# Optimization experiments

Hardware: AMD Instinct MI355X
Metric: run time of the kernel (lower is better)

The kernel has to match this reference:

```python
import jax, jax.numpy as jnp
import numpy as np

D_MODEL = 1024
H = 16
D_K = D_MODEL // H
NEG = -1.0e9


def setup_inputs() -> dict:
    key = jax.random.key(0)
    ks = jax.random.split(key, 12)
    B, S = 2, 2048
    s = 1.0 / np.sqrt(D_MODEL)
    inp = {
        "q": jax.random.normal(ks[0], (B, S, D_MODEL), jnp.float32),
        "k": jax.random.normal(ks[1], (B, S, D_MODEL), jnp.float32),
        "v": jax.random.normal(ks[2], (B, S, D_MODEL), jnp.float32),
        "mask": jnp.tril(jnp.ones((S, S), jnp.int32))[None, None, :, :],
        "wq": jax.random.normal(ks[3], (D_MODEL, D_MODEL), jnp.float32) * s,
        "bq": jax.random.normal(ks[4], (D_MODEL,), jnp.float32) * s,
        "wk": jax.random.normal(ks[5], (D_MODEL, D_MODEL), jnp.float32) * s,
        "bk": jax.random.normal(ks[6], (D_MODEL,), jnp.float32) * s,
        "wv": jax.random.normal(ks[7], (D_MODEL, D_MODEL), jnp.float32) * s,
        "bv": jax.random.normal(ks[8], (D_MODEL,), jnp.float32) * s,
        "wo": jax.random.normal(ks[9], (D_MODEL, D_MODEL), jnp.float32) * s,
        "bo": jax.random.normal(ks[10], (D_MODEL,), jnp.float32) * s,
    }
    return inp


def _split_heads(x):
    # [B,S,D] -> [B,H,S,d_k]
    B, S, _ = x.shape
    return x.reshape(B, S, H, D_K).transpose(0, 2, 1, 3)


def reference(q, k, v, mask, wq, bq, wk, bk, wv, bv, wo, bo):
    # torch Linear: y = x @ W.T + b
    query = _split_heads(q @ wq.T + bq)
    key = _split_heads(k @ wk.T + bk)
    value = _split_heads(v @ wv.T + bv)
    # scores: [B,H,S,S]
    scores = jnp.einsum("bhqd,bhkd->bhqk", query, key) / jnp.sqrt(
        jnp.asarray(D_K, query.dtype))
    scores = jnp.where(mask == 0, jnp.asarray(NEG, scores.dtype), scores)
    attn = jax.nn.softmax(scores, axis=-1)  # dropout p=0.0 -> identity
    x = jnp.einsum("bhqk,bhkd->bhqd", attn, value)
    B, _, S, _ = x.shape
    x = x.transpose(0, 2, 1, 3).reshape(B, S, D_MODEL)
    return x @ wo.T + bo
```

## Files before the change

### kernel.cpp

```cpp
#include <hip/hip_runtime.h>
#include <hip/hip_bf16.h>
#include <cstdint>
#include <cstddef>

#define BATCH 2
#define SEQ   2048
#define DM    1024
#define NH    16
#define DK    64
#define MROWS (BATCH*SEQ)

typedef __bf16 bf16;
typedef float  f32x4  __attribute__((ext_vector_type(4)));
typedef bf16   bf16x8 __attribute__((ext_vector_type(8)));
typedef bf16   bf16x4 __attribute__((ext_vector_type(4)));

#define MFMA32(a, b, c) __builtin_amdgcn_mfma_f32_16x16x32_bf16(a, b, c, 0, 0, 0)

__device__ __forceinline__ void llds16(const void* gc, void* l) {
    void* g = (void*)gc;
    __builtin_amdgcn_global_load_lds(
        (__attribute__((address_space(1))) uint32_t*)g,
        (__attribute__((address_space(3))) uint32_t*)l,
        16, 0, 0);
}

__global__ __launch_bounds__(256) void k_convert(
    const float* __restrict__ q, const float* __restrict__ k, const float* __restrict__ v,
    const float* __restrict__ wq, const float* __restrict__ wk, const float* __restrict__ wv,
    const float* __restrict__ wo,
    bf16* __restrict__ qb, bf16* __restrict__ kb, bf16* __restrict__ vb,
    bf16* __restrict__ wqb, bf16* __restrict__ wkb, bf16* __restrict__ wvb,
    bf16* __restrict__ wob) {
    long t = (long)blockIdx.x * blockDim.x + threadIdx.x;
    const long NQ = (long)MROWS * DM / 4;
    const long NW = (long)DM * DM / 4;
    const float* src; bf16* dst; long off;
    if (t < NQ)            { src = q;  dst = qb;  off = t; }
    else if (t < 2*NQ)     { src = k;  dst = kb;  off = t - NQ; }
    else if (t < 3*NQ)     { src = v;  dst = vb;  off = t - 2*NQ; }
    else {
        long u = t - 3*NQ;
        if (u < NW)        { src = wq; dst = wqb; off = u; }
        else if (u < 2*NW) { src = wk; dst = wkb; off = u - NW; }
        else if (u < 3*NW) { src = wv; dst = wvb; off = u - 2*NW; }
        else               { src = wo; dst = wob; off = u - 3*NW; }
    }
    f32x4 x = *(const f32x4*)(src + off * 4);
    bf16x4 y;
    y[0] = (bf16)x[0]; y[1] = (bf16)x[1]; y[2] = (bf16)x[2]; y[3] = (bf16)x[3];
    *(bf16x4*)(dst + off * 4) = y;
}

__global__ __launch_bounds__(256) void k_gemm_qkv(
    const bf16* __restrict__ qb, const bf16* __restrict__ kb, const bf16* __restrict__ vb,
    const bf16* __restrict__ wqb, const bf16* __restrict__ wkb, const bf16* __restrict__ wvb,
    const float* __restrict__ bq, const float* __restrict__ bk, const float* __restrict__ bv,
    bf16* __restrict__ Qf, bf16* __restrict__ Kf, bf16* __restrict__ Vf) {
    const int z = blockIdx.z;
    const int bid = blockIdx.x;
    const bf16* A; const bf16* B; const float* bias;
    int m0, n0;
    if (z == 2) {
        A = vb; B = wvb; bias = bv;
        m0 = (bid >> 3) * 128;
        n0 = (bid & 7) * 128;
    } else {
        A = z ? wkb : wqb; B = z ? kb : qb; bias = z ? bk : bq;
        m0 = (bid >> 5) * 128;
        n0 = (bid & 31) * 128;
    }

    constexpr int K = DM, BK = 32, NS = K / BK;
    __shared__ bf16 sA[2][128 * BK];
    __shared__ bf16 sB[2][128 * BK];
    const int tid = threadIdx.x;
    const int l = tid & 63, w = tid >> 6;
    const int quad = l >> 4, l15 = l & 15;
    const int wm = w & 1, wn = w >> 1;
    const int srow = l >> 2, scol = (l & 3) * 8;

#pragma unroll
    for (int i = 0; i < 2; ++i) {
        int r16 = w * 32 + i * 16;
        llds16(A + (size_t)(m0 + r16 + srow) * K + scol, &sA[0][r16 * BK]);
        llds16(B + (size_t)(n0 + r16 + srow) * K + scol, &sB[0][r16 * BK]);
    }

    f32x4 acc[4][4] = {};
    for (int s = 0; s < NS; ++s) {
        __syncthreads();
        const int cur = s & 1;
        if (s + 1 < NS) {
            const int k0 = (s + 1) * BK;
#pragma unroll
            for (int i = 0; i < 2; ++i) {
                int r16 = w * 32 + i * 16;
                llds16(A + (size_t)(m0 + r16 + srow) * K + k0 + scol, &sA[cur ^ 1][r16 * BK]);
                llds16(B + (size_t)(n0 + r16 + srow) * K + k0 + scol, &sB[cur ^ 1][r16 * BK]);
            }
        }

        bf16x8 af[4], bfr[4];
#pragma unroll
        for (int mi = 0; mi < 4; ++mi)
            af[mi] = *(const bf16x8*)&sA[cur][(wm * 64 + mi * 16 + l15) * BK + quad * 8];
#pragma unroll
        for (int ni = 0; ni < 4; ++ni)
            bfr[ni] = *(const bf16x8*)&sB[cur][(wn * 64 + ni * 16 + l15) * BK + quad * 8];
#pragma unroll
        for (int mi = 0; mi < 4; ++mi)
#pragma unroll
            for (int ni = 0; ni < 4; ++ni)
                acc[mi][ni] = MFMA32(af[mi], bfr[ni], acc[mi][ni]);
    }

    if (z == 2) {
#pragma unroll
        for (int ni = 0; ni < 4; ++ni) {
            int dcol = n0 + wn * 64 + ni * 16 + l15;
            int hh2 = dcol >> 6;
            int dtile = (dcol >> 4) & 3;
            float bias_v = bias[dcol];
#pragma unroll
            for (int mi = 0; mi < 4; ++mi) {
                int srw = m0 + wm * 64 + mi * 16;
                int bb = srw >> 11, sl = srw & 2047;
                int kc = sl >> 5;
                bf16x4 pack;
#pragma unroll
                for (int r = 0; r < 4; ++r)
                    pack[r] = (bf16)(acc[mi][ni][r] + bias_v);
                size_t entry = ((size_t)(bb * NH + hh2) * 64 + kc) * 4 + dtile;
                *(bf16x4*)(Vf + entry * 512 + (size_t)(quad * 16 + l15) * 8 + (mi & 1) * 4) = pack;
            }
        }
    } else {
        bf16* out = z ? Kf : Qf;
        const float scale = z ? 1.0f : 0.18033688f;
        float bias_rv[4][4];
#pragma unroll
        for (int mi = 0; mi < 4; ++mi)
#pragma unroll
            for (int r = 0; r < 4; ++r)
                bias_rv[mi][r] = bias[m0 + wm * 64 + mi * 16 + quad * 4 + r];
#pragma unroll
        for (int ni = 0; ni < 4; ++ni) {
            int scolg = n0 + wn * 64 + ni * 16 + l15;
            int bb = scolg >> 11, s = scolg & 2047;
            int s16 = s >> 4;
#pragma unroll
            for (int mi = 0; mi < 4; ++mi) {
                int drow = m0 + wm * 64 + mi * 16;
                int hh2 = (drow >> 6) & 15;
                int chunk = (drow & 63) >> 5;
                int qp = 2 * (mi & 1) + (quad >> 1);
                bf16x4 pack;
#pragma unroll
                for (int r = 0; r < 4; ++r)
                    pack[r] = (bf16)((acc[mi][ni][r] + bias_rv[mi][r]) * scale);
                size_t entry = ((size_t)(bb * NH + hh2) * 128 + s16) * 2 + chunk;
                *(bf16x4*)(out + entry * 512 + (size_t)(qp * 16 + l15) * 8 + (quad & 1) * 4) = pack;
            }
        }
    }
}

__global__ __launch_bounds__(256) void k_gemm_out(
    const bf16* __restrict__ X, const bf16* __restrict__ wob,
    const float* __restrict__ bo, float* __restrict__ out) {
    constexpr int K = DM, BK = 32, NS = K / BK;
    const int m0 = blockIdx.y * 128, n0 = blockIdx.x * 128;
    __shared__ bf16 sA[2][128 * BK];
    __shared__ bf16 sB[2][128 * BK];
    const int tid = threadIdx.x;
    const int l = tid & 63, w = tid >> 6;
    const int quad = l >> 4, l15 = l & 15;
    const int wm = w & 1, wn = w >> 1;
    const int srow = l >> 2, scol = (l & 3) * 8;

#pragma unroll
    for (int i = 0; i < 2; ++i) {
        int r16 = w * 32 + i * 16;
        llds16(X + (size_t)(m0 + r16 + srow) * K + scol, &sA[0][r16 * BK]);
        llds16(wob + (size_t)(n0 + r16 + srow) * K + scol, &sB[0][r16 * BK]);
    }

    f32x4 acc[4][4] = {};
    for (int s = 0; s < NS; ++s) {
        __syncthreads();
        const int cur = s & 1;
        if (s + 1 < NS) {
            const int k0 = (s + 1) * BK;
#pragma unroll
            for (int i = 0; i < 2; ++i) {
                int r16 = w * 32 + i * 16;
                llds16(X + (size_t)(m0 + r16 + srow) * K + k0 + scol, &sA[cur ^ 1][r16 * BK]);
                llds16(wob + (size_t)(n0 + r16 + srow) * K + k0 + scol, &sB[cur ^ 1][r16 * BK]);
            }
        }

        bf16x8 af[4], bfr[4];
#pragma unroll
        for (int mi = 0; mi < 4; ++mi)
            af[mi] = *(const bf16x8*)&sA[cur][(wm * 64 + mi * 16 + l15) * BK + quad * 8];
#pragma unroll
        for (int ni = 0; ni < 4; ++ni)
            bfr[ni] = *(const bf16x8*)&sB[cur][(wn * 64 + ni * 16 + l15) * BK + quad * 8];
#pragma unroll
        for (int mi = 0; mi < 4; ++mi)
#pragma unroll
            for (int ni = 0; ni < 4; ++ni)
                acc[mi][ni] = MFMA32(af[mi], bfr[ni], acc[mi][ni]);
    }
#pragma unroll
    for (int mi = 0; mi < 4; ++mi)
#pragma unroll
        for (int ni = 0; ni < 4; ++ni) {
            int col = n0 + wn * 64 + ni * 16 + l15;
            float bias_v = bo[col];
            int rbase = m0 + wm * 64 + mi * 16 + quad * 4;
#pragma unroll
            for (int r = 0; r < 4; ++r)
                out[(size_t)(rbase + r) * DM + col] = acc[mi][ni][r] + bias_v;
        }
}

__global__ __launch_bounds__(256, 4) void k_flash(const bf16* __restrict__ Qf,
                                                  const bf16* __restrict__ Kf,
                                                  const bf16* __restrict__ Vf,
                                                  bf16* __restrict__ X) {
    const int bh = blockIdx.x;
    const int qt = 31 - (int)blockIdx.y;
    const int b = bh >> 4, h = bh & 15;
    const int tid = threadIdx.x, w = tid >> 6, l = tid & 63;
    const int quad = l >> 4, l15 = l & 15;
    __shared__ bf16 sKV[2][16 * 512];

    const bf16* qfp = Qf + (size_t)bh * 128 * 1024;
    const bf16* kfp = Kf + (size_t)bh * 128 * 1024;
    const bf16* vfp = Vf + (size_t)bh * 64 * 4 * 512;

    const int qt16 = qt * 4 + w;
    const int qglob = qt16 * 16 + l15;

    bf16x8 qf[2];
#pragma unroll
    for (int c = 0; c < 2; ++c)
        qf[c] = *(const bf16x8*)(qfp + ((size_t)qt16 * 2 + c) * 512 + (size_t)l * 8);

    f32x4 o[4] = {};
    float lp = 0.f;

#pragma unroll
    for (int i = 0; i < 4; ++i) {
        int e = w * 4 + i;
        const bf16* src = (e < 8) ? kfp + ((size_t)e) * 512
                                  : vfp + ((size_t)(e - 8)) * 512;
        llds16(src + (size_t)l * 8, &sKV[0][e * 512]);
    }

    for (int j = 0; j <= qt; ++j) {
        __syncthreads();
        const bf16* cur = sKV[j & 1];
        if (j < qt) {
            int j1 = j + 1;
#pragma unroll
            for (int i = 0; i < 4; ++i) {
                int e = w * 4 + i;
                const bf16* src = (e < 8) ? kfp + ((size_t)(j1 * 8 + e)) * 512
                                          : vfp + ((size_t)(j1 * 8 + (e - 8))) * 512;
                llds16(src + (size_t)l * 8, (void*)&sKV[j1 & 1][e * 512]);
            }
        }

        f32x4 st[4];
#pragma unroll
        for (int ni = 0; ni < 4; ++ni) {
            bf16x8 k0 = *(const bf16x8*)&cur[(size_t)(ni * 2 + 0) * 512 + l * 8];
            bf16x8 k1 = *(const bf16x8*)&cur[(size_t)(ni * 2 + 1) * 512 + l * 8];
            f32x4 zz = {};
            zz = MFMA32(k0, qf[0], zz);
            st[ni] = MFMA32(k1, qf[1], zz);
        }

        const bool diag = (j == qt);
#pragma unroll
        for (int c = 0; c < 2; ++c) {
            bf16x8 pb;
#pragma unroll
            for (int half = 0; half < 2; ++half) {
                int ni = 2 * c + half;
#pragma unroll
                for (int r = 0; r < 4; ++r) {
                    float s = st[ni][r];
                    if (diag) {
                        int key = j * 64 + ni * 16 + quad * 4 + r;
                        if (key > qglob) s = -1e30f;
                    }
                    float e = __builtin_amdgcn_exp2f(s);
                    lp += e;
                    pb[half * 4 + r] = (bf16)e;
                }
            }
#pragma unroll
            for (int dt = 0; dt < 4; ++dt) {
                bf16x8 vv = *(const bf16x8*)&cur[(size_t)(8 + c * 4 + dt) * 512 + l * 8];
                o[dt] = MFMA32(vv, pb, o[dt]);
            }
        }
    }

    lp += __shfl_xor(lp, 16, 64);
    lp += __shfl_xor(lp, 32, 64);
    float rv = 1.f / lp;

    __syncthreads();
    bf16* Xw = &sKV[0][w * 16 * 72];
#pragma unroll
    for (int dt = 0; dt < 4; ++dt) {
        bf16x4 pk;
#pragma unroll
        for (int r = 0; r < 4; ++r)
            pk[r] = (bf16)(o[dt][r] * rv);
        *(bf16x4*)&Xw[l15 * 72 + dt * 16 + quad * 4] = pk;
    }
#pragma unroll
    for (int i = 0; i < 2; ++i) {
        int row = i * 8 + (l >> 3);
        bf16x8 vv = *(const bf16x8*)&Xw[row * 72 + (l & 7) * 8];
        *(bf16x8*)(X + (size_t)(b * SEQ + qt16 * 16 + row) * DM + h * 64 + (l & 7) * 8) = vv;
    }
}

extern "C" void kernel_launch(void* const* d_in, const int* in_sizes, int n_in,
                              void* d_out, int out_size, void* d_ws, size_t ws_size,
                              hipStream_t stream) {
    const float* q  = (const float*)d_in[0];
    const float* k  = (const float*)d_in[1];
    const float* v  = (const float*)d_in[2];
    const float* wq = (const float*)d_in[4];
    const float* bq = (const float*)d_in[5];
    const float* wk = (const float*)d_in[6];
    const float* bk = (const float*)d_in[7];
    const float* wv = (const float*)d_in[8];
    const float* bv = (const float*)d_in[9];
    const float* wo = (const float*)d_in[10];
    const float* bo = (const float*)d_in[11];
    float* out = (float*)d_out;

    uint8_t* ws = (uint8_t*)d_ws;
    const size_t SZ_ACT = (size_t)MROWS * DM * sizeof(bf16);
    const size_t SZ_W   = (size_t)DM * DM * sizeof(bf16);
    bf16* qb  = (bf16*)(ws);
    bf16* kb  = (bf16*)(ws + SZ_ACT);
    bf16* vb  = (bf16*)(ws + 2 * SZ_ACT);
    bf16* wqb = (bf16*)(ws + 3 * SZ_ACT);
    bf16* wkb = (bf16*)(ws + 3 * SZ_ACT + SZ_W);
    bf16* wvb = (bf16*)(ws + 3 * SZ_ACT + 2 * SZ_W);
    bf16* wob = (bf16*)(ws + 3 * SZ_ACT + 3 * SZ_W);
    bf16* Qf  = (bf16*)(ws + 3 * SZ_ACT + 4 * SZ_W);
    bf16* Kf  = (bf16*)(ws + 4 * SZ_ACT + 4 * SZ_W);
    bf16* Vf  = (bf16*)(ws + 5 * SZ_ACT + 4 * SZ_W);
    bf16* X   = (bf16*)(ws + 6 * SZ_ACT + 4 * SZ_W);

    {
        long total_vec4 = 3L * MROWS * DM / 4 + 4L * DM * DM / 4;
        k_convert<<<dim3((unsigned)(total_vec4 / 256)), 256, 0, stream>>>(
            q, k, v, wq, wk, wv, wo, qb, kb, vb, wqb, wkb, wvb, wob);
    }
    k_gemm_qkv<<<dim3(256, 1, 3), 256, 0, stream>>>(
        qb, kb, vb, wqb, wkb, wvb, bq, bk, bv, Qf, Kf, Vf);
    k_flash<<<dim3(BATCH * NH, SEQ / 64), 256, 0, stream>>>(Qf, Kf, Vf, X);
    k_gemm_out<<<dim3(DM / 128, MROWS / 128), 256, 0, stream>>>(X, wob, bo, out);
}
```

Baseline: 237.6 us.

## Use partial vmcnt waits with raw barriers to overlap async LDS loads

Replaces __syncthreads at the top of each K-step in the projection GEMMs, the output GEMM and the attention loop with an explicit s_waitcnt vmcnt(4) plus s_barrier. The next tile's four global-to-LDS loads can then stay in flight while the current tile is consumed, instead of the full drain that __syncthreads implies. A second barrier after compute guards buffer reuse, and the GEMM address computation is hoisted into incrementing pointers. It also adds a missing __syncthreads before the attention epilogue reads the LDS staging buffer. This relies on hand-counted vmcnt values matching the number of outstanding loads, and adds one extra barrier per iteration.

```diff
diff --git a/kernel.cpp b/kernel.cpp
--- a/kernel.cpp
+++ b/kernel.cpp
@@ -24,6 +24,10 @@
         (__attribute__((address_space(3))) uint32_t*)l,
         16, 0, 0);
 }
+
+#define WAITVM4() asm volatile("s_waitcnt vmcnt(4)" ::: "memory")
+#define WAITVM0() asm volatile("s_waitcnt vmcnt(0)" ::: "memory")
+#define BAR()     __builtin_amdgcn_s_barrier()
 
 __global__ __launch_bounds__(256) void k_convert(
     const float* __restrict__ q, const float* __restrict__ k, const float* __restrict__ v,
@@ -80,27 +84,44 @@
     const int wm = w & 1, wn = w >> 1;
     const int srow = l >> 2, scol = (l & 3) * 8;
 
-#pragma unroll
-    for (int i = 0; i < 2; ++i) {
-        int r16 = w * 32 + i * 16;
-        llds16(A + (size_t)(m0 + r16 + srow) * K + scol, &sA[0][r16 * BK]);
-        llds16(B + (size_t)(n0 + r16 + srow) * K + scol, &sB[0][r16 * BK]);
-    }
+    const int r0 = w * 32, r1 = w * 32 + 16;
+    const bf16* ga0 = A + (size_t)(m0 + r0 + srow) * K + scol;
+    const bf16* ga1 = A + (size_t)(m0 + r1 + srow) * K + scol;
+    const bf16* gb0 = B + (size_t)(n0 + r0 + srow) * K + scol;
+    const bf16* gb1 = B + (size_t)(n0 + r1 + srow) * K + scol;
+    const int la0 = r0 * BK, la1 = r1 * BK;
+
+    llds16(ga0, &sA[0][la0]); llds16(ga1, &sA[0][la1]);
+    llds16(gb0, &sB[0][la0]); llds16(gb1, &sB[0][la1]);
+    ga0 += BK; ga1 += BK; gb0 += BK; gb1 += BK;
 
     f32x4 acc[4][4] = {};
-    for (int s = 0; s < NS; ++s) {
-        __syncthreads();
-        const int cur = s & 1;
-        if (s + 1 < NS) {
-            const int k0 = (s + 1) * BK;
-#pragma unroll
-            for (int i = 0; i < 2; ++i) {
-                int r16 = w * 32 + i * 16;
-                llds16(A + (size_t)(m0 + r16 + srow) * K + k0 + scol, &sA[cur ^ 1][r16 * BK]);
-                llds16(B + (size_t)(n0 + r16 + srow) * K + k0 + scol, &sB[cur ^ 1][r16 * BK]);
-            }
-        }
-
+    for (int s = 0; s < NS - 1; ++s) {
+        const int cur = s & 1, nxt = cur ^ 1;
+        llds16(ga0, &sA[nxt][la0]); llds16(ga1, &sA[nxt][la1]);
+        llds16(gb0, &sB[nxt][la0]); llds16(gb1, &sB[nxt][la1]);
+        ga0 += BK; ga1 += BK; gb0 += BK; gb1 += BK;
+        WAITVM4();
+        BAR();
+
+        bf16x8 af[4], bfr[4];
+#pragma unroll
+        for (int mi = 0; mi < 4; ++mi)
+            af[mi] = *(const bf16x8*)&sA[cur][(wm * 64 + mi * 16 + l15) * BK + quad * 8];
+#pragma unroll
+        for (int ni = 0; ni < 4; ++ni)
+            bfr[ni] = *(const bf16x8*)&sB[cur][(wn * 64 + ni * 16 + l15) * BK + quad * 8];
+#pragma unroll
+        for (int mi = 0; mi < 4; ++mi)
+#pragma unroll
+            for (int ni = 0; ni < 4; ++ni)
+                acc[mi][ni] = MFMA32(af[mi], bfr[ni], acc[mi][ni]);
+        BAR();
+    }
+    {
+        const int cur = (NS - 1) & 1;
+        WAITVM0();
+        BAR();
         bf16x8 af[4], bfr[4];
 #pragma unroll
         for (int mi = 0; mi < 4; ++mi)
@@ -179,27 +200,44 @@
     const int wm = w & 1, wn = w >> 1;
     const int srow = l >> 2, scol = (l & 3) * 8;
 
-#pragma unroll
-    for (int i = 0; i < 2; ++i) {
-        int r16 = w * 32 + i * 16;
-        llds16(X + (size_t)(m0 + r16 + srow) * K + scol, &sA[0][r16 * BK]);
-        llds16(wob + (size_t)(n0 + r16 + srow) * K + scol, &sB[0][r16 * BK]);
-    }
+    const int r0 = w * 32, r1 = w * 32 + 16;
+    const bf16* ga0 = X   + (size_t)(m0 + r0 + srow) * K + scol;
+    const bf16* ga1 = X   + (size_t)(m0 + r1 + srow) * K + scol;
+    const bf16* gb0 = wob + (size_t)(n0 + r0 + srow) * K + scol;
+    const bf16* gb1 = wob + (size_t)(n0 + r1 + srow) * K + scol;
+    const int la0 = r0 * BK, la1 = r1 * BK;
+
+    llds16(ga0, &sA[0][la0]); llds16(ga1, &sA[0][la1]);
+    llds16(gb0, &sB[0][la0]); llds16(gb1, &sB[0][la1]);
+    ga0 += BK; ga1 += BK; gb0 += BK; gb1 += BK;
 
     f32x4 acc[4][4] = {};
-    for (int s = 0; s < NS; ++s) {
-        __syncthreads();
-        const int cur = s & 1;
-        if (s + 1 < NS) {
-            const int k0 = (s + 1) * BK;
-#pragma unroll
-            for (int i = 0; i < 2; ++i) {
-                int r16 = w * 32 + i * 16;
-                llds16(X + (size_t)(m0 + r16 + srow) * K + k0 + scol, &sA[cur ^ 1][r16 * BK]);
-                llds16(wob + (size_t)(n0 + r16 + srow) * K + k0 + scol, &sB[cur ^ 1][r16 * BK]);
-            }
-        }
-
+    for (int s = 0; s < NS - 1; ++s) {
+        const int cur = s & 1, nxt = cur ^ 1;
+        llds16(ga0, &sA[nxt][la0]); llds16(ga1, &sA[nxt][la1]);
+        llds16(gb0, &sB[nxt][la0]); llds16(gb1, &sB[nxt][la1]);
+        ga0 += BK; ga1 += BK; gb0 += BK; gb1 += BK;
+        WAITVM4();
+        BAR();
+
+        bf16x8 af[4], bfr[4];
+#pragma unroll
+        for (int mi = 0; mi < 4; ++mi)
+            af[mi] = *(const bf16x8*)&sA[cur][(wm * 64 + mi * 16 + l15) * BK + quad * 8];
+#pragma unroll
+        for (int ni = 0; ni < 4; ++ni)
+            bfr[ni] = *(const bf16x8*)&sB[cur][(wn * 64 + ni * 16 + l15) * BK + quad * 8];
+#pragma unroll
+        for (int mi = 0; mi < 4; ++mi)
+#pragma unroll
+            for (int ni = 0; ni < 4; ++ni)
+                acc[mi][ni] = MFMA32(af[mi], bfr[ni], acc[mi][ni]);
+        BAR();
+    }
+    {
+        const int cur = (NS - 1) & 1;
+        WAITVM0();
+        BAR();
         bf16x8 af[4], bfr[4];
 #pragma unroll
         for (int mi = 0; mi < 4; ++mi)
@@ -261,7 +299,6 @@
     }
 
     for (int j = 0; j <= qt; ++j) {
-        __syncthreads();
         const bf16* cur = sKV[j & 1];
         if (j < qt) {
             int j1 = j + 1;
@@ -272,7 +309,11 @@
                                           : vfp + ((size_t)(j1 * 8 + (e - 8))) * 512;
                 llds16(src + (size_t)l * 8, (void*)&sKV[j1 & 1][e * 512]);
             }
-        }
+            WAITVM4();
+        } else {
+            WAITVM0();
+        }
+        BAR();
 
         f32x4 st[4];
 #pragma unroll
@@ -309,6 +350,7 @@
                 o[dt] = MFMA32(vv, pb, o[dt]);
             }
         }
+        BAR();
     }
 
     lp += __shfl_xor(lp, 16, 64);
@@ -325,6 +367,7 @@
             pk[r] = (bf16)(o[dt][r] * rv);
         *(bf16x4*)&Xw[l15 * 72 + dt * 16 + quad * 4] = pk;
     }
+    __syncthreads();
 #pragma unroll
     for (int i = 0; i < 2; ++i) {
         int row = i * 8 + (l >> 3);
```

After: 238.2 us. Within noise of the previous version (+0.3%).
